# Performance work log

Hardware: AMD Instinct MI355X
Metric: run time of the kernel (lower is better)

## Reference

```python
import jax, jax.numpy as jnp
import numpy as np

B, D, H = 65536, 128, 64


def setup_inputs() -> dict:
    key = jax.random.key(0)
    ks = jax.random.split(key, 20)
    p = lambda k, shp, fan: jax.random.normal(k, shp, jnp.float32) * (1.0 / np.sqrt(fan))
    return {
        "l": jax.random.normal(ks[0], (B, D), jnp.float32),
        "a": jax.random.normal(ks[1], (B, D), jnp.float32),
        "v": jax.random.normal(ks[2], (B, D), jnp.float32),
        "att_w": p(ks[3], (D, 1), D), "att_b": jnp.zeros((1,), jnp.float32),
        "gf_w1": p(ks[4], (2 * D, H), 2 * D), "gf_b1": jnp.zeros((H,), jnp.float32),
        "gf_w2": p(ks[5], (H, D), H), "gf_b2": jnp.zeros((D,), jnp.float32),
        "gf2_w1": p(ks[6], (2 * D, H), 2 * D), "gf2_b1": jnp.zeros((H,), jnp.float32),
        "gf2_w2": p(ks[7], (H, D), H), "gf2_b2": jnp.zeros((D,), jnp.float32),
        "ll_w1": p(ks[8], (3 * D, H), 3 * D), "ll_b1": jnp.zeros((H,), jnp.float32),
        "ll_w2": p(ks[9], (H, H), H), "ll_b2": jnp.zeros((H,), jnp.float32),
        "ll_w3": p(ks[10], (H, D), H), "ll_b3": jnp.zeros((D,), jnp.float32),
    }


def reference(l, a, v, att_w, att_b, gf_w1, gf_b1, gf_w2, gf_b2,
              gf2_w1, gf2_b1, gf2_w2, gf2_b2,
              ll_w1, ll_b1, ll_w2, ll_b2, ll_w3, ll_b3):
    def gf(x, y):  # graph_fusion on cat([x,y],1): Linear->LeakyReLU(0.2)->Linear->Tanh
        h = jnp.concatenate([x, y], 1) @ gf_w1 + gf_b1
        h = jax.nn.leaky_relu(h, 0.2)
        return jnp.tanh(h @ gf_w2 + gf_b2)

    def gf2(x, y):
        h = jnp.concatenate([x, y], 1) @ gf2_w1 + gf2_b1
        h = jax.nn.leaky_relu(h, 0.2)
        return jnp.tanh(h @ gf2_w2 + gf2_b2)

    dot = lambda x, y: jnp.sum(x * y, axis=1)  # batched [B,1,d]@[B,d,1] -> [B]

    sa = jnp.tanh(a @ att_w + att_b)  # [B,1]
    sv = jnp.tanh(v @ att_w + att_b)
    sl = jnp.tanh(l @ att_w + att_b)

    unimodal = (sa * a + sv * v + sl * l) / 3.0  # [B,D]
    sa1, sv1, sl1 = sa[:, 0], sv[:, 0], sl[:, 0]

    # modalities are overwritten by softmax in the original
    a = jax.nn.softmax(a, axis=1)
    v = jax.nn.softmax(v, axis=1)
    l = jax.nn.softmax(l, axis=1)

    sav = (sa1 + sv1) / (dot(a, v) + 0.5)
    sal = (sa1 + sl1) / (dot(a, l) + 0.5)
    svl = (sl1 + sv1) / (dot(v, l) + 0.5)
    normalize = jax.nn.softmax(jnp.stack([sav, sal, svl], axis=1), axis=1)  # [B,3]

    gav, gal, gvl = gf(a, v), gf(a, l), gf(v, l)  # reused (torch computes twice)
    a_v = jnp.tanh(normalize[:, 0:1] * gav)
    a_l = jnp.tanh(normalize[:, 1:2] * gal)
    v_l = jnp.tanh(normalize[:, 2:3] * gvl)
    bimodal = a_v + a_l + v_l

    a_v2 = jax.nn.softmax(gav, axis=1)
    a_l2 = jax.nn.softmax(gal, axis=1)
    v_l2 = jax.nn.softmax(gvl, axis=1)

    savvl = (sav + svl) / (dot(a_v2, v_l2) + 0.5)
    saavl = (sav + sal) / (dot(a_v2, a_l2) + 0.5)
    savll = (sal + svl) / (dot(a_l2, v_l2) + 0.5)
    savl = (sav + sl1) / (dot(a_v2, l) + 0.5)
    salv = (sal + sv1) / (dot(a_l2, v) + 0.5)
    svla = (sa1 + svl) / (dot(v_l2, a) + 0.5)
    n2 = jax.nn.softmax(jnp.stack([savvl, saavl, savll, savl, salv, svla], axis=1), axis=1)

    trimodal = (jnp.tanh(n2[:, 0:1] * gf2(a_v, v_l))
                + jnp.tanh(n2[:, 1:2] * gf2(a_v, a_l))
                + jnp.tanh(n2[:, 2:3] * gf2(v_l, a_l))
                + jnp.tanh(n2[:, 3:4] * gf2(a_v, l))
                + jnp.tanh(n2[:, 4:5] * gf2(a_l, v))
                + jnp.tanh(n2[:, 5:6] * gf2(v_l, a)))

    fusion = jnp.concatenate([unimodal, bimodal, trimodal], axis=1)  # [B,3D]
    h = jnp.tanh(fusion @ ll_w1 + ll_b1)
    h = jnp.tanh(h @ ll_w2 + ll_b2)
    return jnp.tanh(h @ ll_w3 + ll_b3)
```

## Files before the change

kernel.cpp:

```cpp
#include <hip/hip_runtime.h>

typedef short bfrag __attribute__((ext_vector_type(8)));
typedef float facc  __attribute__((ext_vector_type(4)));
typedef unsigned short u16;
typedef unsigned int   u32;

#define LOG2E 1.4426950408889634f
#define K2E   2.8853900817779268f
#define MFMA(A,B,C) __builtin_amdgcn_mfma_f32_16x16x32_bf16((A),(B),(C),0,0,0)

#define AS_E 0
#define VS_E 2176
#define LS_E 4352
#define AV_E 6528
#define AL_E 8704
#define VL_E 10880
#define HH_E 13056
#define SCR_B 39936
#define SM_BYTES 40704

__device__ __forceinline__ float ex2(float x){ return __builtin_amdgcn_exp2f(x); }
__device__ __forceinline__ float rcpf_(float x){ return __builtin_amdgcn_rcpf(x); }
__device__ __forceinline__ float ftanh_s(float y){ return 1.0f - 2.0f*rcpf_(ex2(y) + 1.0f); }
__device__ __forceinline__ float ftanhb(float y){
  float y2 = y*y, y4 = y2*y2;
  float n = (y2*105.f + 945.f) + y4;
  float d = (y2*420.f + 945.f) + y4*15.f;
  return y*n*rcpf_(d);
}
__device__ __forceinline__ u16 f2b(float x){ return (u16)((__float_as_uint(x) + 0x8000u)>>16); }
__device__ __forceinline__ float b2f(u16 b){ return __uint_as_float(((u32)b)<<16); }
__device__ __forceinline__ u32 pk2(float x0, float x1){
  return __builtin_amdgcn_perm(__float_as_uint(x1)+0x8000u, __float_as_uint(x0)+0x8000u, 0x07060302u);
}
template<int N>
__device__ __forceinline__ float ror16f(float v){
  return __int_as_float(__builtin_amdgcn_update_dpp(0, __float_as_int(v), 0x120|N, 0xF, 0xF, false));
}
__device__ __forceinline__ float rsum16(float v){
  v += ror16f<8>(v); v += ror16f<4>(v); v += ror16f<2>(v); v += ror16f<1>(v); return v;
}
__device__ __forceinline__ void st4b(u16* p, float x0,float x1,float x2,float x3){
  *(uint2*)p = make_uint2(pk2(x0,x1), pk2(x2,x3));
}

__global__ void prep_weights(const float* __restrict__ gf_w1, const float* __restrict__ gf_w2,
                             const float* __restrict__ gf2_w1, const float* __restrict__ gf2_w2,
                             const float* __restrict__ ll_w1, const float* __restrict__ ll_w2,
                             const float* __restrict__ ll_w3, u16* __restrict__ blob)
{
  u32 i = blockIdx.x*256u + threadIdx.x;
  if (i >= 86016u) return;
  u32 off, K, ln; const float* src;
  if      (i < 16384u){ off=0u;     K=256u; ln=6u; src=gf_w1; }
  else if (i < 24576u){ off=16384u; K=64u;  ln=7u; src=gf_w2; }
  else if (i < 40960u){ off=24576u; K=256u; ln=6u; src=gf2_w1; }
  else if (i < 49152u){ off=40960u; K=64u;  ln=7u; src=gf2_w2; }
  else if (i < 73728u){ off=49152u; K=384u; ln=6u; src=ll_w1; }
  else if (i < 77824u){ off=73728u; K=64u;  ln=6u; src=ll_w2; }
  else               { off=77824u; K=64u;  ln=7u; src=ll_w3; }
  u32 li = i - off;
  u32 k = li >> ln, n = li & ((1u<<ln)-1u);
  blob[off + n*K + k] = f2b(src[li]);
}

__global__ __launch_bounds__(256,4) void fused_graph(
    const float* __restrict__ Lg, const float* __restrict__ Ag, const float* __restrict__ Vg,
    const float* __restrict__ att_w, const float* __restrict__ att_b,
    const float* __restrict__ gf_b1, const float* __restrict__ gf_b2,
    const float* __restrict__ gf2_b1, const float* __restrict__ gf2_b2,
    const float* __restrict__ ll_b1, const float* __restrict__ ll_b2, const float* __restrict__ ll_b3,
    const u16* __restrict__ wb, float* __restrict__ out)
{
  __shared__ alignas(16) char sm[SM_BYTES];
  u16* smu = (u16*)sm;
  float* scr = (float*)(sm + SCR_B);

  const int tid = threadIdx.x;
  const int lane = tid & 63;
  const int w = tid >> 6;
  const int m = lane & 15;
  const int q = lane >> 4;
  const int er = tid >> 4;
  const int ep = tid & 15;
  const int row0 = blockIdx.x << 4;

  const int gb = (row0 + er)*128 + ep*4;
  facc A0 = *(const facc*)(Ag+gb), A1 = *(const facc*)(Ag+gb+64);
  facc V0 = *(const facc*)(Vg+gb), V1 = *(const facc*)(Vg+gb+64);
  facc L0 = *(const facc*)(Lg+gb), L1 = *(const facc*)(Lg+gb+64);
  facc W0 = *(const facc*)(att_w+ep*4), W1 = *(const facc*)(att_w+ep*4+64);
  float abK = att_b[0]*K2E;
  float pa=0.f,pv=0.f,pl=0.f;
  #pragma unroll
  for (int i=0;i<4;i++){ pa += A0[i]*W0[i]+A1[i]*W1[i]; pv += V0[i]*W0[i]+V1[i]*W1[i]; pl += L0[i]*W0[i]+L1[i]*W1[i]; }
  float sa = ftanh_s(rsum16(pa)*K2E + abK);
  float sv = ftanh_s(rsum16(pv)*K2E + abK);
  float sl = ftanh_s(rsum16(pl)*K2E + abK);
  u32 uni_pk[4];
  {
    const float th = 1.0f/3.0f;
    uni_pk[0] = pk2((sa*A0[0]+sv*V0[0]+sl*L0[0])*th, (sa*A0[1]+sv*V0[1]+sl*L0[1])*th);
    uni_pk[1] = pk2((sa*A0[2]+sv*V0[2]+sl*L0[2])*th, (sa*A0[3]+sv*V0[3]+sl*L0[3])*th);
    uni_pk[2] = pk2((sa*A1[0]+sv*V1[0]+sl*L1[0])*th, (sa*A1[1]+sv*V1[1]+sl*L1[1])*th);
    uni_pk[3] = pk2((sa*A1[2]+sv*V1[2]+sl*L1[2])*th, (sa*A1[3]+sv*V1[3]+sl*L1[3])*th);
  }
  #define SMAX(X0,X1,OFFE) { \
    float s_=0.f; \
    _Pragma("unroll") for (int i=0;i<4;i++){ X0[i]=ex2(X0[i]*LOG2E); X1[i]=ex2(X1[i]*LOG2E); s_+=X0[i]+X1[i]; } \
    s_ = rsum16(s_); float rs_ = rcpf_(s_); \
    _Pragma("unroll") for (int i=0;i<4;i++){ X0[i]*=rs_; X1[i]*=rs_; } \
    u16* dp_ = smu + (OFFE) + er*136 + ep*4; \
    st4b(dp_, X0[0],X0[1],X0[2],X0[3]); st4b(dp_+64, X1[0],X1[1],X1[2],X1[3]); }
  SMAX(A0,A1,AS_E)
  SMAX(V0,V1,VS_E)
  SMAX(L0,L1,LS_E)
  float dav=0.f,dal=0.f,dvl=0.f;
  #pragma unroll
  for (int i=0;i<4;i++){ dav += A0[i]*V0[i]+A1[i]*V1[i]; dal += A0[i]*L0[i]+A1[i]*L1[i]; dvl += V0[i]*L0[i]+V1[i]*L1[i]; }
  dav = rsum16(dav); dal = rsum16(dal); dvl = rsum16(dvl);
  float sav = (sa+sv)*rcpf_(dav+0.5f);
  float sal = (sa+sl)*rcpf_(dal+0.5f);
  float svl = (sl+sv)*rcpf_(dvl+0.5f);
  if (ep==0){
    float e0 = ex2(sav*LOG2E), e1 = ex2(sal*LOG2E), e2 = ex2(svl*LOG2E);
    float rs = rcpf_(e0+e1+e2);
    scr[er*12+0]=e0*rs; scr[er*12+1]=e1*rs; scr[er*12+2]=e2*rs;
  }
  __syncthreads();

  const u16* g1t = wb;
  const u16* g2t = wb + 16384;
  bfrag B1[8];
  #pragma unroll
  for (int s=0;s<8;s++) B1[s] = *(const bfrag*)(g1t + (w*16+m)*256 + s*32 + q*8);
  facc acc0={0,0,0,0}, acc1={0,0,0,0}, acc2={0,0,0,0};
  #pragma unroll
  for (int s=0;s<8;s++){
    int k = s*32 + q*8, ko = k & 127; bool hi = (k >= 128);
    const u16* p0 = smu + (hi? VS_E:AS_E) + m*136 + ko;
    const u16* p1 = smu + (hi? LS_E:AS_E) + m*136 + ko;
    const u16* p2 = smu + (hi? LS_E:VS_E) + m*136 + ko;
    acc0 = MFMA(*(const bfrag*)p0, B1[s], acc0);
    acc1 = MFMA(*(const bfrag*)p1, B1[s], acc1);
    acc2 = MFMA(*(const bfrag*)p2, B1[s], acc2);
  }
  {
    float b1v = gf_b1[w*16+m];
    #pragma unroll
    for (int r=0;r<4;r++){
      int rr = q*4+r;
      float h0 = acc0[r]+b1v; h0 = fmaxf(h0, 0.2f*h0);
      float h1 = acc1[r]+b1v; h1 = fmaxf(h1, 0.2f*h1);
      float h2 = acc2[r]+b1v; h2 = fmaxf(h2, 0.2f*h2);
      smu[HH_E + 0*1152 + rr*72 + w*16+m] = f2b(h0);
      smu[HH_E + 1*1152 + rr*72 + w*16+m] = f2b(h1);
      smu[HH_E + 2*1152 + rr*72 + w*16+m] = f2b(h2);
    }
  }
  __syncthreads();
  facc c2[3][2] = {{{0,0,0,0},{0,0,0,0}},{{0,0,0,0},{0,0,0,0}},{{0,0,0,0},{0,0,0,0}}};
  #pragma unroll
  for (int s=0;s<2;s++){
    int k = s*32 + q*8;
    bfrag Af0 = *(const bfrag*)(smu + HH_E + 0*1152 + m*72 + k);
    bfrag Af1 = *(const bfrag*)(smu + HH_E + 1*1152 + m*72 + k);
    bfrag Af2 = *(const bfrag*)(smu + HH_E + 2*1152 + m*72 + k);
    #pragma unroll
    for (int t=0;t<2;t++){
      bfrag B2f = *(const bfrag*)(g2t + ((w+4*t)*16+m)*64 + s*32 + q*8);
      c2[0][t] = MFMA(Af0, B2f, c2[0][t]);
      c2[1][t] = MFMA(Af1, B2f, c2[1][t]);
      c2[2][t] = MFMA(Af2, B2f, c2[2][t]);
    }
  }
  {
    float b2v0s = gf_b2[w*16+m]*K2E, b2v1s = gf_b2[(w+4)*16+m]*K2E;
    #pragma unroll
    for (int p3=0;p3<3;p3++){
      #pragma unroll
      for (int t=0;t<2;t++){
        float bbs = t? b2v1s : b2v0s;
        int cc = (w+4*t)*16+m;
        #pragma unroll
        for (int r=0;r<4;r++){
          smu[AV_E + p3*2176 + (q*4+r)*136 + cc] = f2b(ftanh_s(c2[p3][t][r]*K2E + bbs));
        }
      }
    }
  }
  __syncthreads();

  float E0[8], E1[8], E2[8], bim8[8];
  float RS0, RS1, RS2;
  #pragma unroll
  for (int j=0;j<8;j++) bim8[j]=0.f;
  #define GSTATC(EA, G3, RS) { \
    u16* gpa_ = smu + AV_E + (G3)*2176 + er*136 + ep*4; \
    u16* gpb_ = gpa_ + 64; \
    ushort4 ga_ = *(const ushort4*)gpa_; ushort4 gb_ = *(const ushort4*)gpb_; \
    float x_[8]; \
    x_[0]=b2f(ga_.x); x_[1]=b2f(ga_.y); x_[2]=b2f(ga_.z); x_[3]=b2f(ga_.w); \
    x_[4]=b2f(gb_.x); x_[5]=b2f(gb_.y); x_[6]=b2f(gb_.z); x_[7]=b2f(gb_.w); \
    float nn_ = scr[er*12+(G3)]; \
    float t_[8]; \
    _Pragma("unroll") for (int j=0;j<8;j++){ t_[j]=ftanhb(nn_*x_[j]); bim8[j]+=t_[j]; } \
    st4b(gpa_, t_[0],t_[1],t_[2],t_[3]); \
    st4b(gpb_, t_[4],t_[5],t_[6],t_[7]); \
    float s_=0.f; \
    _Pragma("unroll") for (int j=0;j<8;j++){ x_[j]=ex2(x_[j]*LOG2E); s_+=x_[j]; } \
    s_ = rsum16(s_); RS = rcpf_(s_); \
    _Pragma("unroll") for (int j=0;j<8;j++) EA[j]=x_[j]; }
  GSTATC(E0,0,RS0)
  GSTATC(E1,1,RS1)
  GSTATC(E2,2,RS2)
  float d01=0.f,d02=0.f,d12=0.f,d0l=0.f,d1v=0.f,d2a=0.f;
  #pragma unroll
  for (int i=0;i<4;i++){
    d01 += E0[i]*E1[i] + E0[4+i]*E1[4+i];
    d02 += E0[i]*E2[i] + E0[4+i]*E2[4+i];
    d12 += E1[i]*E2[i] + E1[4+i]*E2[4+i];
    d0l += E0[i]*L0[i] + E0[4+i]*L1[i];
    d1v += E1[i]*V0[i] + E1[4+i]*V1[i];
    d2a += E2[i]*A0[i] + E2[4+i]*A1[i];
  }
  d01=rsum16(d01)*(RS0*RS1); d02=rsum16(d02)*(RS0*RS2); d12=rsum16(d12)*(RS1*RS2);
  d0l=rsum16(d0l)*RS0;       d1v=rsum16(d1v)*RS1;       d2a=rsum16(d2a)*RS2;
  if (ep==0){
    float x0 = (sav+svl)*rcpf_(d02+0.5f);
    float x1 = (sav+sal)*rcpf_(d01+0.5f);
    float x2 = (sal+svl)*rcpf_(d12+0.5f);
    float x3 = (sav+sl )*rcpf_(d0l+0.5f);
    float x4 = (sal+sv )*rcpf_(d1v+0.5f);
    float x5 = (sa +svl)*rcpf_(d2a+0.5f);
    float e0=ex2(x0*LOG2E), e1=ex2(x1*LOG2E), e2=ex2(x2*LOG2E);
    float e3=ex2(x3*LOG2E), e4=ex2(x4*LOG2E), e5=ex2(x5*LOG2E);
    float rs = rcpf_(e0+e1+e2+e3+e4+e5);
    scr[er*12+4]=e0*rs; scr[er*12+5]=e1*rs; scr[er*12+6]=e2*rs;
    scr[er*12+7]=e3*rs; scr[er*12+8]=e4*rs; scr[er*12+9]=e5*rs;
  }
  __syncthreads();

  const u16* h1t = wb + 24576;
  const u16* h2t = wb + 40960;
  bfrag C1[8];
  #pragma unroll
  for (int s=0;s<8;s++) C1[s] = *(const bfrag*)(h1t + (w*16+m)*256 + s*32 + q*8);
  const int S0[6] = {AV_E, AV_E, VL_E, AV_E, AL_E, VL_E};
  const int S1[6] = {VL_E, AL_E, AL_E, LS_E, VS_E, AS_E};
  facc cc1[6];
  #pragma unroll
  for (int pr=0;pr<6;pr++){ facc z = {0,0,0,0}; cc1[pr] = z; }
  #pragma unroll
  for (int s=0;s<8;s++){
    int k = s*32+q*8, ko = k&127; bool hi = (k>=128);
    #pragma unroll
    for (int pr=0;pr<6;pr++){
      const u16* sp = smu + (hi? S1[pr]:S0[pr]) + m*136 + ko;
      cc1[pr] = MFMA(*(const bfrag*)sp, C1[s], cc1[pr]);
    }
  }
  {
    float b1v = gf2_b1[w*16+m];
    #pragma unroll
    for (int pr=0;pr<6;pr++){
      #pragma unroll
      for (int r=0;r<4;r++){
        float h = cc1[pr][r]+b1v; h = fmaxf(h,0.2f*h);
        smu[HH_E + pr*1152 + (q*4+r)*72 + w*16+m] = f2b(h);
      }
    }
  }
  __syncthreads();
  facc cc2[6][2];
  #pragma unroll
  for (int pr=0;pr<6;pr++){ facc z = {0,0,0,0}; cc2[pr][0]=z; cc2[pr][1]=z; }
  #pragma unroll
  for (int s=0;s<2;s++){
    int k=s*32+q*8;
    bfrag Af[6];
    #pragma unroll
    for (int pr=0;pr<6;pr++) Af[pr] = *(const bfrag*)(smu + HH_E + pr*1152 + m*72 + k);
    #pragma unroll
    for (int t=0;t<2;t++){
      bfrag C2f = *(const bfrag*)(h2t + ((w+4*t)*16+m)*64 + s*32 + q*8);
      #pragma unroll
      for (int pr=0;pr<6;pr++) cc2[pr][t] = MFMA(Af[pr], C2f, cc2[pr][t]);
    }
  }
  {
    float b2v0s = gf2_b2[w*16+m]*K2E, b2v1s = gf2_b2[(w+4)*16+m]*K2E;
    float tri[2][4] = {{0,0,0,0},{0,0,0,0}};
    float n2v[4][6];
    #pragma unroll
    for (int r=0;r<4;r++){
      const float4 v4 = *(const float4*)(scr + (q*4+r)*12 + 4);
      const float2 v2 = *(const float2*)(scr + (q*4+r)*12 + 8);
      n2v[r][0]=v4.x; n2v[r][1]=v4.y; n2v[r][2]=v4.z; n2v[r][3]=v4.w;
      n2v[r][4]=v2.x; n2v[r][5]=v2.y;
    }
    #pragma unroll
    for (int pr=0;pr<6;pr++){
      #pragma unroll
      for (int t=0;t<2;t++){
        float bbs = t? b2v1s : b2v0s;
        #pragma unroll
        for (int r=0;r<4;r++){
          float g = ftanh_s(cc2[pr][t][r]*K2E + bbs);
          tri[t][r] += ftanhb(n2v[r][pr]*g);
        }
      }
    }
    #pragma unroll
    for (int t=0;t<2;t++){
      #pragma unroll
      for (int r=0;r<4;r++){
        smu[LS_E + (q*4+r)*136 + (w+4*t)*16+m] = f2b(tri[t][r]);
      }
    }
    u16* vp = smu + VS_E + er*136 + ep*4;
    st4b(vp,    bim8[0],bim8[1],bim8[2],bim8[3]);
    st4b(vp+64, bim8[4],bim8[5],bim8[6],bim8[7]);
    *(uint2*)(smu + AS_E + er*136 + ep*4)      = make_uint2(uni_pk[0], uni_pk[1]);
    *(uint2*)(smu + AS_E + er*136 + ep*4 + 64) = make_uint2(uni_pk[2], uni_pk[3]);
  }
  __syncthreads();

  const u16* lw1 = wb + 49152;
  const u16* lw2 = wb + 73728;
  const u16* lw3 = wb + 77824;
  {
    facc c = {0,0,0,0};
    #pragma unroll
    for (int s=0;s<12;s++){
      const int base = (s<4)? AS_E : (s<8)? VS_E : LS_E;
      bfrag Bf = *(const bfrag*)(lw1 + (w*16+m)*384 + s*32 + q*8);
      bfrag Af = *(const bfrag*)(smu + base + m*136 + (s&3)*32 + q*8);
      c = MFMA(Af, Bf, c);
    }
    float bs = ll_b1[w*16+m]*K2E;
    #pragma unroll
    for (int r=0;r<4;r++) smu[HH_E + (q*4+r)*72 + w*16+m] = f2b(ftanh_s(c[r]*K2E + bs));
  }
  __syncthreads();
  {
    facc c = {0,0,0,0};
    #pragma unroll
    for (int s=0;s<2;s++){
      bfrag Bf = *(const bfrag*)(lw2 + (w*16+m)*64 + s*32 + q*8);
      bfrag Af = *(const bfrag*)(smu + HH_E + m*72 + s*32 + q*8);
      c = MFMA(Af, Bf, c);
    }
    float bs = ll_b2[w*16+m]*K2E;
    #pragma unroll
    for (int r=0;r<4;r++) smu[HH_E + 1152 + (q*4+r)*72 + w*16+m] = f2b(ftanh_s(c[r]*K2E + bs));
  }
  __syncthreads();
  {
    facc c0={0,0,0,0}, c1={0,0,0,0};
    #pragma unroll
    for (int s=0;s<2;s++){
      bfrag Af  = *(const bfrag*)(smu + HH_E + 1152 + m*72 + s*32 + q*8);
      bfrag Bf0 = *(const bfrag*)(lw3 + (w*16+m)*64 + s*32 + q*8);
      bfrag Bf1 = *(const bfrag*)(lw3 + ((w+4)*16+m)*64 + s*32 + q*8);
      c0 = MFMA(Af, Bf0, c0);
      c1 = MFMA(Af, Bf1, c1);
    }
    float b0s = ll_b3[w*16+m]*K2E, b1s = ll_b3[(w+4)*16+m]*K2E;
    #pragma unroll
    for (int r=0;r<4;r++){
      out[(row0+q*4+r)*128 + w*16+m]        = ftanh_s(c0[r]*K2E + b0s);
      out[(row0+q*4+r)*128 + (w+4)*16+m]    = ftanh_s(c1[r]*K2E + b1s);
    }
  }
}

extern "C" void kernel_launch(void* const* d_in, const int* in_sizes, int n_in,
                              void* d_out, int out_size, void* d_ws, size_t ws_size,
                              hipStream_t stream)
{
  const float* l      = (const float*)d_in[0];
  const float* a      = (const float*)d_in[1];
  const float* v      = (const float*)d_in[2];
  const float* att_w  = (const float*)d_in[3];
  const float* att_b  = (const float*)d_in[4];
  const float* gf_w1  = (const float*)d_in[5];
  const float* gf_b1  = (const float*)d_in[6];
  const float* gf_w2  = (const float*)d_in[7];
  const float* gf_b2  = (const float*)d_in[8];
  const float* gf2_w1 = (const float*)d_in[9];
  const float* gf2_b1 = (const float*)d_in[10];
  const float* gf2_w2 = (const float*)d_in[11];
  const float* gf2_b2 = (const float*)d_in[12];
  const float* ll_w1  = (const float*)d_in[13];
  const float* ll_b1  = (const float*)d_in[14];
  const float* ll_w2  = (const float*)d_in[15];
  const float* ll_b2  = (const float*)d_in[16];
  const float* ll_w3  = (const float*)d_in[17];
  const float* ll_b3  = (const float*)d_in[18];
  u16* blob = (u16*)d_ws;

  prep_weights<<<336, 256, 0, stream>>>(gf_w1, gf_w2, gf2_w1, gf2_w2, ll_w1, ll_w2, ll_w3, blob);
  fused_graph<<<4096, 256, 0, stream>>>(l, a, v, att_w, att_b,
                                        gf_b1, gf_b2, gf2_b1, gf2_b2,
                                        ll_b1, ll_b2, ll_b3, blob, (float*)d_out);
}
```

Before: 245.6 us.

## Reassign MLP stages per wave to drop intra-block barriers

In the graph-fusion stage, waves 0–2 each now compute one whole modality pair (both Linear layers) on their own, and wave 3 sits idle there. This removes the barrier between the two layers. In the final three-layer MLP, every wave computes the full first and second hidden layers redundantly into a private LDS slice. That removes two more __syncthreads, and the last layer stays split across waves. The cost is more total MFMA work and more weight loads (4x redundant for ll1/ll2) plus load imbalance, in exchange for fewer block-wide synchronisations.

```diff
diff --git a/kernel.cpp b/kernel.cpp
--- a/kernel.cpp
+++ b/kernel.cpp
@@ -131,61 +131,45 @@
 
   const u16* g1t = wb;
   const u16* g2t = wb + 16384;
-  bfrag B1[8];
-  #pragma unroll
-  for (int s=0;s<8;s++) B1[s] = *(const bfrag*)(g1t + (w*16+m)*256 + s*32 + q*8);
-  facc acc0={0,0,0,0}, acc1={0,0,0,0}, acc2={0,0,0,0};
-  #pragma unroll
-  for (int s=0;s<8;s++){
-    int k = s*32 + q*8, ko = k & 127; bool hi = (k >= 128);
-    const u16* p0 = smu + (hi? VS_E:AS_E) + m*136 + ko;
-    const u16* p1 = smu + (hi? LS_E:AS_E) + m*136 + ko;
-    const u16* p2 = smu + (hi? LS_E:VS_E) + m*136 + ko;
-    acc0 = MFMA(*(const bfrag*)p0, B1[s], acc0);
-    acc1 = MFMA(*(const bfrag*)p1, B1[s], acc1);
-    acc2 = MFMA(*(const bfrag*)p2, B1[s], acc2);
-  }
-  {
-    float b1v = gf_b1[w*16+m];
-    #pragma unroll
-    for (int r=0;r<4;r++){
-      int rr = q*4+r;
-      float h0 = acc0[r]+b1v; h0 = fmaxf(h0, 0.2f*h0);
-      float h1 = acc1[r]+b1v; h1 = fmaxf(h1, 0.2f*h1);
-      float h2 = acc2[r]+b1v; h2 = fmaxf(h2, 0.2f*h2);
-      smu[HH_E + 0*1152 + rr*72 + w*16+m] = f2b(h0);
-      smu[HH_E + 1*1152 + rr*72 + w*16+m] = f2b(h1);
-      smu[HH_E + 2*1152 + rr*72 + w*16+m] = f2b(h2);
-    }
-  }
-  __syncthreads();
-  facc c2[3][2] = {{{0,0,0,0},{0,0,0,0}},{{0,0,0,0},{0,0,0,0}},{{0,0,0,0},{0,0,0,0}}};
-  #pragma unroll
-  for (int s=0;s<2;s++){
-    int k = s*32 + q*8;
-    bfrag Af0 = *(const bfrag*)(smu + HH_E + 0*1152 + m*72 + k);
-    bfrag Af1 = *(const bfrag*)(smu + HH_E + 1*1152 + m*72 + k);
-    bfrag Af2 = *(const bfrag*)(smu + HH_E + 2*1152 + m*72 + k);
-    #pragma unroll
-    for (int t=0;t<2;t++){
-      bfrag B2f = *(const bfrag*)(g2t + ((w+4*t)*16+m)*64 + s*32 + q*8);
-      c2[0][t] = MFMA(Af0, B2f, c2[0][t]);
-      c2[1][t] = MFMA(Af1, B2f, c2[1][t]);
-      c2[2][t] = MFMA(Af2, B2f, c2[2][t]);
-    }
-  }
-  {
-    float b2v0s = gf_b2[w*16+m]*K2E, b2v1s = gf_b2[(w+4)*16+m]*K2E;
-    #pragma unroll
-    for (int p3=0;p3<3;p3++){
-      #pragma unroll
-      for (int t=0;t<2;t++){
-        float bbs = t? b2v1s : b2v0s;
-        int cc = (w+4*t)*16+m;
-        #pragma unroll
-        for (int r=0;r<4;r++){
-          smu[AV_E + p3*2176 + (q*4+r)*136 + cc] = f2b(ftanh_s(c2[p3][t][r]*K2E + bbs));
-        }
+  if (w < 3){
+    const int XO = (w==2)? VS_E : AS_E;
+    const int YO = (w==0)? VS_E : LS_E;
+    bfrag Afr[8];
+    #pragma unroll
+    for (int s=0;s<8;s++){
+      int k = s*32 + q*8, ko = k & 127;
+      Afr[s] = *(const bfrag*)(smu + ((k>=128)? YO : XO) + m*136 + ko);
+    }
+    #pragma unroll
+    for (int tt=0;tt<4;tt++){
+      facc c = {0,0,0,0};
+      #pragma unroll
+      for (int s=0;s<8;s++){
+        bfrag Bf = *(const bfrag*)(g1t + (tt*16+m)*256 + s*32 + q*8);
+        c = MFMA(Afr[s], Bf, c);
+      }
+      float b1v = gf_b1[tt*16+m];
+      #pragma unroll
+      for (int r=0;r<4;r++){
+        float h = c[r]+b1v; h = fmaxf(h, 0.2f*h);
+        smu[HH_E + w*1152 + (q*4+r)*72 + tt*16+m] = f2b(h);
+      }
+    }
+    bfrag A2[2];
+    #pragma unroll
+    for (int s=0;s<2;s++) A2[s] = *(const bfrag*)(smu + HH_E + w*1152 + m*72 + s*32 + q*8);
+    #pragma unroll
+    for (int tt=0;tt<8;tt++){
+      facc c = {0,0,0,0};
+      #pragma unroll
+      for (int s=0;s<2;s++){
+        bfrag Bf = *(const bfrag*)(g2t + (tt*16+m)*64 + s*32 + q*8);
+        c = MFMA(A2[s], Bf, c);
+      }
+      float bbs = gf_b2[tt*16+m]*K2E;
+      #pragma unroll
+      for (int r=0;r<4;r++){
+        smu[AV_E + w*2176 + (q*4+r)*136 + tt*16+m] = f2b(ftanh_s(c[r]*K2E + bbs));
       }
     }
   }
@@ -330,47 +314,62 @@
   const u16* lw2 = wb + 73728;
   const u16* lw3 = wb + 77824;
   {
-    facc c = {0,0,0,0};
+    bfrag Afu[12];
     #pragma unroll
     for (int s=0;s<12;s++){
       const int base = (s<4)? AS_E : (s<8)? VS_E : LS_E;
-      bfrag Bf = *(const bfrag*)(lw1 + (w*16+m)*384 + s*32 + q*8);
-      bfrag Af = *(const bfrag*)(smu + base + m*136 + (s&3)*32 + q*8);
-      c = MFMA(Af, Bf, c);
-    }
-    float bs = ll_b1[w*16+m]*K2E;
-    #pragma unroll
-    for (int r=0;r<4;r++) smu[HH_E + (q*4+r)*72 + w*16+m] = f2b(ftanh_s(c[r]*K2E + bs));
-  }
-  __syncthreads();
-  {
-    facc c = {0,0,0,0};
+      Afu[s] = *(const bfrag*)(smu + base + m*136 + (s&3)*32 + q*8);
+    }
+    #pragma unroll
+    for (int tt=0;tt<4;tt++){
+      facc c = {0,0,0,0};
+      #pragma unroll
+      for (int s=0;s<12;s++){
+        bfrag Bf = *(const bfrag*)(lw1 + (tt*16+m)*384 + s*32 + q*8);
+        c = MFMA(Afu[s], Bf, c);
+      }
+      float bs = ll_b1[tt*16+m]*K2E;
+      #pragma unroll
+      for (int r=0;r<4;r++)
+        smu[HH_E + w*1152 + (q*4+r)*72 + tt*16+m] = f2b(ftanh_s(c[r]*K2E + bs));
+    }
+    bfrag Ah[2];
+    #pragma unroll
+    for (int s=0;s<2;s++) Ah[s] = *(const bfrag*)(smu + HH_E + w*1152 + m*72 + s*32 + q*8);
+    facc ch[4];
+    #pragma unroll
+    for (int tt=0;tt<4;tt++){
+      facc c = {0,0,0,0};
+      #pragma unroll
+      for (int s=0;s<2;s++){
+        bfrag Bf = *(const bfrag*)(lw2 + (tt*16+m)*64 + s*32 + q*8);
+        c = MFMA(Ah[s], Bf, c);
+      }
+      ch[tt] = c;
+    }
+    #pragma unroll
+    for (int tt=0;tt<4;tt++){
+      float bs = ll_b2[tt*16+m]*K2E;
+      #pragma unroll
+      for (int r=0;r<4;r++)
+        smu[HH_E + w*1152 + (q*4+r)*72 + tt*16+m] = f2b(ftanh_s(ch[tt][r]*K2E + bs));
+    }
+    bfrag Ah2[2];
+    #pragma unroll
+    for (int s=0;s<2;s++) Ah2[s] = *(const bfrag*)(smu + HH_E + w*1152 + m*72 + s*32 + q*8);
+    facc c0={0,0,0,0}, c1={0,0,0,0};
     #pragma unroll
     for (int s=0;s<2;s++){
-      bfrag Bf = *(const bfrag*)(lw2 + (w*16+m)*64 + s*32 + q*8);
-      bfrag Af = *(const bfrag*)(smu + HH_E + m*72 + s*32 + q*8);
-      c = MFMA(Af, Bf, c);
-    }
-    float bs = ll_b2[w*16+m]*K2E;
-    #pragma unroll
-    for (int r=0;r<4;r++) smu[HH_E + 1152 + (q*4+r)*72 + w*16+m] = f2b(ftanh_s(c[r]*K2E + bs));
-  }
-  __syncthreads();
-  {
-    facc c0={0,0,0,0}, c1={0,0,0,0};
-    #pragma unroll
-    for (int s=0;s<2;s++){
-      bfrag Af  = *(const bfrag*)(smu + HH_E + 1152 + m*72 + s*32 + q*8);
       bfrag Bf0 = *(const bfrag*)(lw3 + (w*16+m)*64 + s*32 + q*8);
       bfrag Bf1 = *(const bfrag*)(lw3 + ((w+4)*16+m)*64 + s*32 + q*8);
-      c0 = MFMA(Af, Bf0, c0);
-      c1 = MFMA(Af, Bf1, c1);
+      c0 = MFMA(Ah2[s], Bf0, c0);
+      c1 = MFMA(Ah2[s], Bf1, c1);
     }
     float b0s = ll_b3[w*16+m]*K2E, b1s = ll_b3[(w+4)*16+m]*K2E;
     #pragma unroll
     for (int r=0;r<4;r++){
-      out[(row0+q*4+r)*128 + w*16+m]        = ftanh_s(c0[r]*K2E + b0s);
-      out[(row0+q*4+r)*128 + (w+4)*16+m]    = ftanh_s(c1[r]*K2E + b1s);
+      out[(row0+q*4+r)*128 + w*16+m]     = ftanh_s(c0[r]*K2E + b0s);
+      out[(row0+q*4+r)*128 + (w+4)*16+m] = ftanh_s(c1[r]*K2E + b1s);
     }
   }
 }
```

Measured after the change: 367.8 us. 1.5x slower.
